# Kernel optimization log

Measured on AMD Instinct MI355X. Metric: run time of the kernel, lower is better.

The kernel has to match this reference:

```python
import jax, jax.numpy as jnp
import numpy as np

N_NODES = 10000
N_EDGES = 160000
MUL = 128            # channel multiplicity of node features
N_ELEM = 10          # node_attrs scalars (num elements)
N_EDGE_FEATS = 8     # radial basis size
W_NUMEL = 4 * MUL    # 4 uvu paths, 128 weights each
AVG_NEIGH = 16.0
INV_SQRT3 = 0.5773502691896258  # CG coefficient for 1o x 1o -> 0e (dot product path)


def setup_inputs() -> dict:
    key = jax.random.key(0)
    ks = jax.random.split(key, 12)
    node_attrs = jax.random.uniform(ks[0], (N_NODES, N_ELEM), dtype=jnp.float32)
    node_feats = jax.random.normal(ks[1], (N_NODES, MUL * 4), dtype=jnp.float32)  # 128x0e + 128x1o flattened
    edge_attrs = jax.random.normal(ks[2], (N_EDGES, 4), dtype=jnp.float32)        # Y0 (1) + Y1 (3)
    edge_feats = jax.random.normal(ks[3], (N_EDGES, N_EDGE_FEATS), dtype=jnp.float32)
    edge_index = jax.random.randint(ks[4], (2, N_EDGES), 0, N_NODES, dtype=jnp.int64)
    # learned parameters (xavier-ish scales; e3nn path norms folded into weights)
    W_up0 = jax.random.normal(ks[5], (MUL, MUL), dtype=jnp.float32) / np.sqrt(MUL)
    W_up1 = jax.random.normal(ks[6], (MUL, MUL), dtype=jnp.float32) / np.sqrt(MUL)
    W_tpw = jax.random.normal(ks[7], (N_ELEM, N_EDGE_FEATS, W_NUMEL), dtype=jnp.float32) / np.sqrt(N_ELEM * N_EDGE_FEATS)
    W_lin0 = jax.random.normal(ks[8], (2 * MUL, MUL), dtype=jnp.float32) / np.sqrt(2 * MUL)
    W_lin1 = jax.random.normal(ks[9], (2 * MUL, MUL), dtype=jnp.float32) / np.sqrt(2 * MUL)
    W_sk0 = jax.random.normal(ks[10], (MUL, N_ELEM, MUL), dtype=jnp.float32) / np.sqrt(MUL * N_ELEM)
    W_sk1 = jax.random.normal(ks[11], (MUL, N_ELEM, MUL), dtype=jnp.float32) / np.sqrt(MUL * N_ELEM)
    return dict(node_attrs=node_attrs, node_feats=node_feats, edge_attrs=edge_attrs,
                edge_feats=edge_feats, edge_index=edge_index,
                W_up0=W_up0, W_up1=W_up1, W_tpw=W_tpw,
                W_lin0=W_lin0, W_lin1=W_lin1, W_sk0=W_sk0, W_sk1=W_sk1)


def reference(node_attrs, node_feats, edge_attrs, edge_feats, edge_index,
              W_up0, W_up1, W_tpw, W_lin0, W_lin1, W_sk0, W_sk1):
    N = node_feats.shape[0]
    sender, receiver = edge_index[0], edge_index[1]
    x0 = node_feats[:, :MUL]                       # [N,128] scalars (0e)
    x1 = node_feats[:, MUL:].reshape(N, MUL, 3)    # [N,128,3] vectors (1o)

    # skip_tp: FullyConnectedTensorProduct(node_feats, node_attrs -> 128x0e+128x1o)
    sc0 = jnp.einsum('nu,na,uak->nk', x0, node_attrs, W_sk0)        # [N,128]
    sc1 = jnp.einsum('num,na,uak->nkm', x1, node_attrs, W_sk1)      # [N,128,3]

    # linear_up: per-l linear
    h0 = x0 @ W_up0                                   # [N,128]
    h1 = jnp.einsum('num,uk->nkm', x1, W_up1)         # [N,128,3]

    # per-edge TP weights: einsum('be,ba,aek->bk')
    tpw = jnp.einsum('be,ba,aek->bk', edge_feats, node_attrs[sender], W_tpw)  # [E,512]
    w1, w2, w3, w4 = tpw[:, :MUL], tpw[:, MUL:2*MUL], tpw[:, 2*MUL:3*MUL], tpw[:, 3*MUL:]

    Y0 = edge_attrs[:, 0]       # [E]
    Y1 = edge_attrs[:, 1:4]     # [E,3]
    hs0 = h0[sender]            # [E,128] gather
    hs1 = h1[sender]            # [E,128,3]

    # conv_tp (uvu, external per-edge weights), 4 CG paths:
    m0a = w1 * hs0 * Y0[:, None]                                       # 0e x 0e -> 0e
    m1a = (w2 * hs0)[:, :, None] * Y1[:, None, :]                      # 0e x 1o -> 1o
    m1b = hs1 * (w3 * Y0[:, None])[:, :, None]                         # 1o x 0e -> 1o
    m0b = w4 * (INV_SQRT3 * jnp.einsum('eum,em->eu', hs1, Y1))         # 1o x 1o -> 0e
    m0 = jnp.concatenate([m0a, m0b], axis=1)    # [E,256]  irreps_mid 0e block
    m1 = jnp.concatenate([m1a, m1b], axis=1)    # [E,256,3] irreps_mid 1o block

    # scatter_sum over receiver
    msg0 = jax.ops.segment_sum(m0, receiver, num_segments=N)   # [N,256]
    msg1 = jax.ops.segment_sum(m1, receiver, num_segments=N)   # [N,256,3]

    # linear (irreps_mid -> 128x0e+128x1o) / avg_num_neighbors + skip
    out0 = (msg0 @ W_lin0) / AVG_NEIGH + sc0                        # [N,128]
    out1 = jnp.einsum('num,uk->nkm', msg1, W_lin1) / AVG_NEIGH + sc1  # [N,128,3]
    return jnp.concatenate([out0, out1.reshape(N, MUL * 3)], axis=1)  # [N,512]
```

## Files before the change

kernel.cpp:

```cpp
#include <hip/hip_runtime.h>

#define NN 10000
#define NE 160000
#define NBK0 157
#define NBK1 469

constexpr float INV_AVG = 1.0f / 16.0f;
constexpr float INV_SQRT3F = 0.5773502691896258f;

typedef __attribute__((ext_vector_type(8))) short short8v;
typedef __attribute__((ext_vector_type(8))) unsigned short ushort8v;
typedef __attribute__((ext_vector_type(4))) float float4v;

#define OF_UP0 0
#define OF_UP1 16384
#define OF_SK0 32768
#define OF_SK1 196608
#define OF_LN0 360448
#define OF_LN1 393216
#define WPK_TOT 425984
#define WTP_TOT 49152

__device__ __forceinline__ unsigned short f2bf(float f) {
    unsigned int u = __float_as_uint(f);
    return (unsigned short)((u + 0x7FFFu + ((u >> 16) & 1u)) >> 16);
}
__device__ __forceinline__ float bf2f(unsigned short h) {
    return __uint_as_float(((unsigned int)h) << 16);
}

__global__ __launch_bounds__(256) void prep_w_kernel(
    const float* __restrict__ W_up0, const float* __restrict__ W_up1,
    const float* __restrict__ W_sk0, const float* __restrict__ W_sk1,
    const float* __restrict__ W_lin0, const float* __restrict__ W_lin1,
    unsigned short* __restrict__ wpk)
{
    const int g = blockIdx.x * 256 + threadIdx.x;
    if (g >= WPK_TOT / 8) return;
    const float* src; int local, base; bool sk = false;
    if (g < 2048)       { src = W_up0;  local = g;         base = OF_UP0; }
    else if (g < 4096)  { src = W_up1;  local = g - 2048;  base = OF_UP1; }
    else if (g < 24576) { src = W_sk0;  local = g - 4096;  base = OF_SK0; sk = true; }
    else if (g < 45056) { src = W_sk1;  local = g - 24576; base = OF_SK1; sk = true; }
    else if (g < 49152) { src = W_lin0; local = g - 45056; base = OF_LN0; }
    else                { src = W_lin1; local = g - 49152; base = OF_LN1; }
    const int k8 = local >> 7, n = local & 127;
    ushort8v v;
    #pragma unroll
    for (int j = 0; j < 8; ++j) {
        const int k = k8 * 8 + j;
        int row;
        if (sk) {
            const int a = k >> 7, u = k & 127;
            row = u * 10 + a;
        } else {
            row = k;
        }
        v[j] = f2bf(src[(size_t)row * 128 + n]);
    }
    *(ushort8v*)(wpk + (size_t)base + (size_t)local * 8) = v;
}

__global__ __launch_bounds__(256) void prep_wt_kernel(
    const float* __restrict__ W_tpw, unsigned short* __restrict__ wtp)
{
    const int g = blockIdx.x * 256 + threadIdx.x;
    if (g >= 6144) return;
    const int k8 = g >> 9, col = g & 511;
    ushort8v v;
    #pragma unroll
    for (int j = 0; j < 8; ++j) {
        const int k = k8 * 8 + j;
        v[j] = (k < 80) ? f2bf(W_tpw[(size_t)k * 512 + col]) : (unsigned short)0;
    }
    *(ushort8v*)(wtp + (size_t)g * 8) = v;
}

__global__ __launch_bounds__(256, 2) void node_mfma_kernel(
    const float* __restrict__ node_attrs,
    const float* __restrict__ node_feats,
    const unsigned short* __restrict__ wpk,
    float* __restrict__ hbuf,
    float* __restrict__ out)
{
    __shared__ __align__(16) unsigned short habuf[1024][8];
    __shared__ __align__(16) unsigned short bbuf[2][1024][8];
    __shared__ float atrow[64][10];

    const int t = threadIdx.x;
    const int bid = blockIdx.x;
    const bool m1 = (bid >= NBK0);
    const int r0 = m1 ? (bid - NBK0) * 64 : bid * 64;
    const int RTOT = m1 ? 30000 : 10000;

    const unsigned short* __restrict__ wup = wpk + (m1 ? OF_UP1 : OF_UP0);
    const unsigned short* __restrict__ wsk = wpk + (m1 ? OF_SK1 : OF_SK0);

    const int rg_ = t >> 2, pg_ = t & 3;
    const int rr_g = min(r0 + rg_, RTOT - 1);
    int n_g, m_g;
    if (!m1) { n_g = rr_g; m_g = 0; }
    else     { n_g = rr_g / 3; m_g = rr_g - n_g * 3; }
    const int wq = rg_ >> 4, rlq = rg_ & 15;

    #pragma unroll
    for (int q = 0; q < 4; ++q) {
        const int sl = pg_ * 4 + q, ss = sl >> 2, kb = sl & 3;
        const int k0 = ss * 32 + kb * 8;
        ushort8v v;
        if (!m1) {
            const float4 xa_ = *(const float4*)(node_feats + (size_t)n_g * 512 + k0);
            const float4 xb_ = *(const float4*)(node_feats + (size_t)n_g * 512 + k0 + 4);
            v[0] = f2bf(xa_.x); v[1] = f2bf(xa_.y); v[2] = f2bf(xa_.z); v[3] = f2bf(xa_.w);
            v[4] = f2bf(xb_.x); v[5] = f2bf(xb_.y); v[6] = f2bf(xb_.z); v[7] = f2bf(xb_.w);
        } else {
            #pragma unroll
            for (int j = 0; j < 8; ++j)
                v[j] = f2bf(node_feats[(size_t)n_g * 512 + 128 + (k0 + j) * 3 + m_g]);
        }
        *(ushort8v*)&habuf[((ss * 4 + wq) * 4 + kb) * 16 + rlq][0] = v;
    }
    for (int i = t; i < 640; i += 256) {
        const int r = i / 10, a = i - r * 10;
        const int rr = min(r0 + r, RTOT - 1);
        const int n = m1 ? (rr / 3) : rr;
        atrow[r][a] = node_attrs[n * 10 + a];
    }
    __syncthreads();

    const int w = t >> 6, lane = t & 63;
    const int rl = lane & 15, kq = lane >> 4;

    {
        float4v hacc[8];
        #pragma unroll
        for (int nt = 0; nt < 8; ++nt) hacc[nt] = (float4v){0.f, 0.f, 0.f, 0.f};

        #pragma unroll
        for (int ss = 0; ss < 4; ++ss) {
            const short8v af = *(const short8v*)&habuf[((ss * 4 + w) * 4 + kq) * 16 + rl][0];
            #pragma unroll
            for (int nt = 0; nt < 8; ++nt) {
                const short8v bf = *(const short8v*)(wup +
                    ((size_t)((ss * 4 + kq) * 128 + nt * 16 + rl)) * 8);
                hacc[nt] = __builtin_amdgcn_mfma_f32_16x16x32_bf16(af, bf, hacc[nt], 0, 0, 0);
            }
        }
        #pragma unroll
        for (int nt = 0; nt < 8; ++nt)
            #pragma unroll
            for (int v2 = 0; v2 < 4; ++v2) {
                const int rr = r0 + w * 16 + kq * 4 + v2;
                if (rr < RTOT) {
                    const int col = nt * 16 + rl;
                    if (!m1) hbuf[(size_t)rr * 512 + col] = hacc[nt][v2];
                    else {
                        const int n = rr / 3, m = rr - n * 3;
                        hbuf[(size_t)n * 512 + 128 + m * 128 + col] = hacc[nt][v2];
                    }
                }
            }
    }

    float4v sacc[8];
    #pragma unroll
    for (int nt = 0; nt < 8; ++nt) sacc[nt] = (float4v){0.f, 0.f, 0.f, 0.f};

    #pragma unroll
    for (int i = 0; i < 4; ++i) {
        const int s = i * 256 + t;
        const int ssb = s >> 9, ntb = (s >> 6) & 7, kbb = (s >> 4) & 3, nlb = s & 15;
        const int k8 = ssb * 4 + kbb;
        const int n = ntb * 16 + nlb;
        *(ushort8v*)&bbuf[0][s][0] =
            *(const ushort8v*)(wsk + ((size_t)(k8 * 128 + n)) * 8);
    }
    __syncthreads();

    int cur = 0;
    for (int ks = 0; ks < 20; ++ks) {
        ushort8v tmp[4];
        if (ks < 19) {
            #pragma unroll
            for (int i = 0; i < 4; ++i) {
                const int s = i * 256 + t;
                const int ssb = s >> 9, ntb = (s >> 6) & 7, kbb = (s >> 4) & 3, nlb = s & 15;
                const int k8 = (ks + 1) * 8 + ssb * 4 + kbb;
                const int n = ntb * 16 + nlb;
                tmp[i] = *(const ushort8v*)(wsk + ((size_t)(k8 * 128 + n)) * 8);
            }
        }

        short8v af[2];
        #pragma unroll
        for (int ss = 0; ss < 2; ++ss) {
            const int kp = ks * 64 + ss * 32 + kq * 8;
            const int a = kp >> 7, u0 = kp & 127;
            const ushort8v xh = *(const ushort8v*)&habuf[
                (((u0 >> 5) * 4 + w) * 4 + ((u0 >> 3) & 3)) * 16 + rl][0];
            const float av = atrow[w * 16 + rl][a];
            ushort8v vv;
            #pragma unroll
            for (int j = 0; j < 8; ++j) vv[j] = f2bf(bf2f(xh[j]) * av);
            af[ss] = (short8v)vv;
        }

        #pragma unroll
        for (int ss = 0; ss < 2; ++ss)
            #pragma unroll
            for (int nt = 0; nt < 8; ++nt) {
                const short8v bf =
                    *(const short8v*)&bbuf[cur][((ss * 8 + nt) * 4 + kq) * 16 + rl][0];
                sacc[nt] = __builtin_amdgcn_mfma_f32_16x16x32_bf16(af[ss], bf, sacc[nt], 0, 0, 0);
            }

        if (ks < 19) {
            #pragma unroll
            for (int i = 0; i < 4; ++i) {
                const int s = i * 256 + t;
                *(ushort8v*)&bbuf[cur ^ 1][s][0] = tmp[i];
            }
        }
        __syncthreads();
        cur ^= 1;
    }

    #pragma unroll
    for (int nt = 0; nt < 8; ++nt)
        #pragma unroll
        for (int v2 = 0; v2 < 4; ++v2) {
            const int rr = r0 + w * 16 + kq * 4 + v2;
            if (rr < RTOT) {
                const int col = nt * 16 + rl;
                if (!m1) out[(size_t)rr * 512 + col] = sacc[nt][v2];
                else {
                    const int n = rr / 3, m = rr - n * 3;
                    out[(size_t)n * 512 + 128 + col * 3 + m] = sacc[nt][v2];
                }
            }
        }
}

__global__ __launch_bounds__(256) void hist_kernel(
    const int* __restrict__ recv, int* __restrict__ cnt)
{
    const int e = blockIdx.x * 256 + threadIdx.x;
    if (e < NE) atomicAdd(&cnt[recv[e]], 1);
}

__global__ __launch_bounds__(256) void scan_kernel(
    const int* __restrict__ cnt, int* __restrict__ row_start,
    int* __restrict__ head)
{
    __shared__ int part[256];
    const int t = threadIdx.x;
    const int base = t * 40;
    int s = 0;
    if (base < NN)
        for (int b = 0; b < 40; ++b) s += cnt[base + b];
    part[t] = s;
    __syncthreads();
    const int local = s;
    for (int off = 1; off < 256; off <<= 1) {
        const int v = (t >= off) ? part[t - off] : 0;
        __syncthreads();
        part[t] += v;
        __syncthreads();
    }
    const int excl = part[t] - local;
    if (base < NN) {
        int run = excl;
        for (int b = 0; b < 40; ++b) {
            row_start[base + b] = run;
            head[base + b] = run;
            run += cnt[base + b];
        }
    }
    if (t == 0) row_start[NN] = NE;
}

__global__ __launch_bounds__(256) void scatter_kernel(
    const int* __restrict__ recv, int* __restrict__ head,
    int* __restrict__ elist)
{
    const int e = blockIdx.x * 256 + threadIdx.x;
    if (e < NE) {
        const int p = atomicAdd(&head[recv[e]], 1);
        elist[p] = e;
    }
}

__global__ __launch_bounds__(256) void pack2_kernel(
    const float* __restrict__ node_attrs,
    const float* __restrict__ edge_attrs,
    const float* __restrict__ edge_feats,
    const int*  __restrict__ edge_index,
    const int*  __restrict__ elist,
    unsigned short* __restrict__ zpk,
    float* __restrict__ ypk)
{
    const int pos = blockIdx.x * 256 + threadIdx.x;
    if (pos >= NE) return;
    const int e = elist[pos];
    const int snd = edge_index[e];

    float ef[8];
    *(float4*)&ef[0] = *(const float4*)(edge_feats + (size_t)e * 8);
    *(float4*)&ef[4] = *(const float4*)(edge_feats + (size_t)e * 8 + 4);
    float at[10];
    #pragma unroll
    for (int a = 0; a < 10; ++a) at[a] = node_attrs[(size_t)snd * 10 + a];

    #pragma unroll
    for (int k8 = 0; k8 < 12; ++k8) {
        ushort8v v;
        #pragma unroll
        for (int j = 0; j < 8; ++j) {
            const int A = k8 * 8 + j;
            const float z = (A < 80) ? at[A >> 3] * ef[A & 7] : 0.f;
            v[j] = f2bf(z);
        }
        *(ushort8v*)(zpk + ((size_t)k8 * NE + pos) * 8) = v;
    }

    const float4 ea = *(const float4*)(edge_attrs + (size_t)e * 4);
    *(float4*)(ypk + (size_t)pos * 8) = ea;
    *(float4*)(ypk + (size_t)pos * 8 + 4) =
        make_float4(__int_as_float(snd), 0.f, 0.f, 0.f);
}

__global__ __launch_bounds__(256, 2) void gather_mfma_kernel(
    const unsigned short* __restrict__ wtp,
    const float* __restrict__ hbuf,
    const int*  __restrict__ row_start,
    const unsigned short* __restrict__ zpk,
    const float* __restrict__ ypk,
    float* __restrict__ msgbuf)
{
    __shared__ __align__(16) unsigned short zb[384][8];
    __shared__ float yb[32][9];

    const int t = threadIdx.x;
    const int p = blockIdx.x & 1;
    const int ngrp = blockIdx.x >> 1;
    const int w = t >> 6, lane = t & 63;
    const int rl = lane & 15, kq = lane >> 4;

    short8v breg[2][3][2];
    #pragma unroll
    for (int wi = 0; wi < 2; ++wi)
        #pragma unroll
        for (int ks = 0; ks < 3; ++ks)
            #pragma unroll
            for (int ct = 0; ct < 2; ++ct) {
                const int col = p * 256 + wi * 128 + w * 32 + ct * 16 + rl;
                breg[wi][ks][ct] = *(const short8v*)(wtp +
                    ((size_t)((ks * 4 + kq) * 512 + col)) * 8);
            }

    for (int nn = 0; nn < 4; ++nn) {
        const int node = ngrp * 4 + nn;
        const int rowst = row_start[node];
        const int deg = row_start[node + 1] - rowst;

        float nacc[2][4];
        #pragma unroll
        for (int ct = 0; ct < 2; ++ct)
            #pragma unroll
            for (int j = 0; j < 4; ++j) nacc[ct][j] = 0.f;

        for (int ce = 0; ce < deg; ce += 32) {
            const int cl = min(32, deg - ce);
            __syncthreads();

            {
                const int s = t;
                const int rl2 = s & 15, kq2 = (s >> 4) & 3;
                const int rowt2 = (s >> 6) & 1, ks2 = s >> 7;
                const int e = rowt2 * 16 + rl2;
                const int k8 = ks2 * 4 + kq2;
                ushort8v v = {0, 0, 0, 0, 0, 0, 0, 0};
                if (e < cl)
                    v = *(const ushort8v*)(zpk + ((size_t)k8 * NE + rowst + ce + e) * 8);
                *(ushort8v*)&zb[s][0] = v;
            }
            {
                const int s = 256 + t;
                if (s < 384) {
                    const int rl2 = s & 15, kq2 = (s >> 4) & 3;
                    const int rowt2 = (s >> 6) & 1, ks2 = s >> 7;
                    const int e = rowt2 * 16 + rl2;
                    const int k8 = ks2 * 4 + kq2;
                    ushort8v v = {0, 0, 0, 0, 0, 0, 0, 0};
                    if (e < cl)
                        v = *(const ushort8v*)(zpk + ((size_t)k8 * NE + rowst + ce + e) * 8);
                    *(ushort8v*)&zb[s][0] = v;
                }
            }
            if (t < 64) {
                const int row = t >> 1, half = t & 1;
                float4 v = make_float4(0.f, 0.f, 0.f, 0.f);
                if (row < cl)
                    v = *(const float4*)(ypk + (size_t)(rowst + ce + row) * 8 + half * 4);
                yb[row][half * 4 + 0] = v.x;
                yb[row][half * 4 + 1] = v.y;
                yb[row][half * 4 + 2] = v.z;
                yb[row][half * 4 + 3] = v.w;
            }
            __syncthreads();

            if (p == 0) {
                #pragma unroll
                for (int rt = 0; rt < 2; ++rt) {
                    if (rt == 1 && cl <= 16) continue;
                    float h0v[4][2];
                    #pragma unroll
                    for (int v = 0; v < 4; ++v) {
                        const int e = rt * 16 + kq * 4 + v;
                        const int snd = __float_as_int(yb[e][4]);
                        const float* hrow = hbuf + (size_t)snd * 512;
                        #pragma unroll
                        for (int ct = 0; ct < 2; ++ct)
                            h0v[v][ct] = hrow[w * 32 + ct * 16 + rl];
                    }
                    float4v acc[2][2];
                    #pragma unroll
                    for (int wi = 0; wi < 2; ++wi)
                        #pragma unroll
                        for (int ct = 0; ct < 2; ++ct)
                            acc[wi][ct] = (float4v){0.f, 0.f, 0.f, 0.f};
                    #pragma unroll
                    for (int ks = 0; ks < 3; ++ks) {
                        const short8v af =
                            *(const short8v*)&zb[ks * 128 + rt * 64 + lane][0];
                        #pragma unroll
                        for (int wi = 0; wi < 2; ++wi)
                            #pragma unroll
                            for (int ct = 0; ct < 2; ++ct)
                                acc[wi][ct] = __builtin_amdgcn_mfma_f32_16x16x32_bf16(
                                    af, breg[wi][ks][ct], acc[wi][ct], 0, 0, 0);
                    }
                    #pragma unroll
                    for (int v = 0; v < 4; ++v) {
                        const int e = rt * 16 + kq * 4 + v;
                        const float Y0  = yb[e][0];
                        const float Y10 = yb[e][1];
                        const float Y11 = yb[e][2];
                        const float Y12 = yb[e][3];
                        #pragma unroll
                        for (int ct = 0; ct < 2; ++ct) {
                            const float tA = acc[0][ct][v];
                            const float tB = acc[1][ct][v];
                            const float h0 = h0v[v][ct];
                            nacc[ct][0] = fmaf(tA * Y0, h0, nacc[ct][0]);
                            const float tm = tB * h0;
                            nacc[ct][1] = fmaf(tm, Y10, nacc[ct][1]);
                            nacc[ct][2] = fmaf(tm, Y11, nacc[ct][2]);
                            nacc[ct][3] = fmaf(tm, Y12, nacc[ct][3]);
                        }
                    }
                }
            } else {
                #pragma unroll
                for (int rt = 0; rt < 2; ++rt) {
                    if (rt == 1 && cl <= 16) continue;
                    float hA[4][2], hB[4][2], hC[4][2];
                    #pragma unroll
                    for (int v = 0; v < 4; ++v) {
                        const int e = rt * 16 + kq * 4 + v;
                        const int snd = __float_as_int(yb[e][4]);
                        const float* hrow = hbuf + (size_t)snd * 512;
                        #pragma unroll
                        for (int ct = 0; ct < 2; ++ct) {
                            const int c = w * 32 + ct * 16 + rl;
                            hA[v][ct] = hrow[128 + c];
                            hB[v][ct] = hrow[256 + c];
                            hC[v][ct] = hrow[384 + c];
                        }
                    }
                    float4v acc[2][2];
                    #pragma unroll
                    for (int wi = 0; wi < 2; ++wi)
                        #pragma unroll
                        for (int ct = 0; ct < 2; ++ct)
                            acc[wi][ct] = (float4v){0.f, 0.f, 0.f, 0.f};
                    #pragma unroll
                    for (int ks = 0; ks < 3; ++ks) {
                        const short8v af =
                            *(const short8v*)&zb[ks * 128 + rt * 64 + lane][0];
                        #pragma unroll
                        for (int wi = 0; wi < 2; ++wi)
                            #pragma unroll
                            for (int ct = 0; ct < 2; ++ct)
                                acc[wi][ct] = __builtin_amdgcn_mfma_f32_16x16x32_bf16(
                                    af, breg[wi][ks][ct], acc[wi][ct], 0, 0, 0);
                    }
                    #pragma unroll
                    for (int v = 0; v < 4; ++v) {
                        const int e = rt * 16 + kq * 4 + v;
                        const float Y0  = yb[e][0];
                        const float Y10 = yb[e][1];
                        const float Y11 = yb[e][2];
                        const float Y12 = yb[e][3];
                        #pragma unroll
                        for (int ct = 0; ct < 2; ++ct) {
                            const float tA = acc[0][ct][v];
                            const float tB = acc[1][ct][v];
                            const float t2 = tA * Y0;
                            nacc[ct][1] = fmaf(t2, hA[v][ct], nacc[ct][1]);
                            nacc[ct][2] = fmaf(t2, hB[v][ct], nacc[ct][2]);
                            nacc[ct][3] = fmaf(t2, hC[v][ct], nacc[ct][3]);
                            float d = hA[v][ct] * Y10;
                            d = fmaf(hB[v][ct], Y11, d);
                            d = fmaf(hC[v][ct], Y12, d);
                            nacc[ct][0] = fmaf(tB * INV_SQRT3F, d, nacc[ct][0]);
                        }
                    }
                }
            }
        }

        float red[2][4];
        #pragma unroll
        for (int ct = 0; ct < 2; ++ct)
            #pragma unroll
            for (int j = 0; j < 4; ++j) {
                float v = nacc[ct][j];
                v += __shfl_xor(v, 16, 64);
                v += __shfl_xor(v, 32, 64);
                red[ct][j] = v;
            }
        if (kq == 0) {
            float* mrow = msgbuf + (size_t)node * 1024;
            #pragma unroll
            for (int ct = 0; ct < 2; ++ct) {
                const int c = w * 32 + ct * 16 + rl;
                if (p == 0) {
                    mrow[c]       = red[ct][0];
                    mrow[256 + c] = red[ct][1];
                    mrow[512 + c] = red[ct][2];
                    mrow[768 + c] = red[ct][3];
                } else {
                    mrow[128 + c] = red[ct][0];
                    mrow[384 + c] = red[ct][1];
                    mrow[640 + c] = red[ct][2];
                    mrow[896 + c] = red[ct][3];
                }
            }
        }
    }
}

__global__ __launch_bounds__(256, 2) void out_mfma_kernel(
    const float* __restrict__ msgbuf,
    const unsigned short* __restrict__ wpk,
    float* __restrict__ out)
{
    __shared__ __align__(16) unsigned short habuf[2048][8];

    const int t = threadIdx.x;
    const int n0 = blockIdx.x * 16;

    const int rg_ = t >> 2, pg_ = t & 3;
    const int wq = rg_ >> 4, rlq = rg_ & 15;
    const float* src = msgbuf + (size_t)(n0 + rlq) * 1024 + wq * 256;

    #pragma unroll
    for (int q = 0; q < 8; ++q) {
        const int sl = pg_ * 8 + q, ss = sl >> 2, kb = sl & 3;
        const int k0 = ss * 32 + kb * 8;
        const float4 xa = *(const float4*)(src + k0);
        const float4 xb = *(const float4*)(src + k0 + 4);
        ushort8v v;
        v[0] = f2bf(xa.x); v[1] = f2bf(xa.y); v[2] = f2bf(xa.z); v[3] = f2bf(xa.w);
        v[4] = f2bf(xb.x); v[5] = f2bf(xb.y); v[6] = f2bf(xb.z); v[7] = f2bf(xb.w);
        *(ushort8v*)&habuf[((ss * 4 + wq) * 4 + kb) * 16 + rlq][0] = v;
    }
    __syncthreads();

    const int w = t >> 6, lane = t & 63;
    const int rl = lane & 15, kq = lane >> 4;
    const unsigned short* __restrict__ wl = wpk + ((w == 0) ? OF_LN0 : OF_LN1);

    float4v acc[8];
    #pragma unroll
    for (int nt = 0; nt < 8; ++nt) acc[nt] = (float4v){0.f, 0.f, 0.f, 0.f};

    #pragma unroll
    for (int ss = 0; ss < 8; ++ss) {
        const short8v af = *(const short8v*)&habuf[((ss * 4 + w) * 4 + kq) * 16 + rl][0];
        #pragma unroll
        for (int nt = 0; nt < 8; ++nt) {
            const short8v bf = *(const short8v*)(wl +
                ((size_t)((ss * 4 + kq) * 128 + nt * 16 + rl)) * 8);
            acc[nt] = __builtin_amdgcn_mfma_f32_16x16x32_bf16(af, bf, acc[nt], 0, 0, 0);
        }
    }

    #pragma unroll
    for (int nt = 0; nt < 8; ++nt)
        #pragma unroll
        for (int v2 = 0; v2 < 4; ++v2) {
            const int n = n0 + kq * 4 + v2;
            const int col = nt * 16 + rl;
            if (w == 0) {
                out[(size_t)n * 512 + col] += acc[nt][v2] * INV_AVG;
            } else {
                const int m = w - 1;
                out[(size_t)n * 512 + 128 + col * 3 + m] += acc[nt][v2] * INV_AVG;
            }
        }
}

extern "C" void kernel_launch(void* const* d_in, const int* in_sizes, int n_in,
                              void* d_out, int out_size, void* d_ws, size_t ws_size,
                              hipStream_t stream) {
    const float* node_attrs = (const float*)d_in[0];
    const float* node_feats = (const float*)d_in[1];
    const float* edge_attrs = (const float*)d_in[2];
    const float* edge_feats = (const float*)d_in[3];
    const int*   edge_index = (const int*)d_in[4];
    const float* W_up0  = (const float*)d_in[5];
    const float* W_up1  = (const float*)d_in[6];
    const float* W_tpw  = (const float*)d_in[7];
    const float* W_lin0 = (const float*)d_in[8];
    const float* W_lin1 = (const float*)d_in[9];
    const float* W_sk0  = (const float*)d_in[10];
    const float* W_sk1  = (const float*)d_in[11];
    float* out = (float*)d_out;

    float* hbuf   = (float*)d_ws;
    float* msgbuf = hbuf + (size_t)NN * 512;
    float* ypk    = msgbuf + (size_t)NN * 1024;
    unsigned short* zpk = (unsigned short*)(ypk + (size_t)NE * 8);
    unsigned short* wpk = zpk + (size_t)12 * NE * 8;
    unsigned short* wtp = wpk + WPK_TOT;
    int* cnt       = (int*)(wtp + WTP_TOT);
    int* row_start = cnt + NN;
    int* head      = row_start + NN + 1;
    int* elist     = head + NN;

    const int* recv = edge_index + NE;

    hipMemsetAsync(cnt, 0, NN * sizeof(int), stream);
    hist_kernel<<<(NE + 255) / 256, 256, 0, stream>>>(recv, cnt);
    scan_kernel<<<1, 256, 0, stream>>>(cnt, row_start, head);
    scatter_kernel<<<(NE + 255) / 256, 256, 0, stream>>>(recv, head, elist);
    pack2_kernel<<<(NE + 255) / 256, 256, 0, stream>>>(
        node_attrs, edge_attrs, edge_feats, edge_index, elist, zpk, ypk);
    prep_w_kernel<<<(WPK_TOT / 8 + 255) / 256, 256, 0, stream>>>(
        W_up0, W_up1, W_sk0, W_sk1, W_lin0, W_lin1, wpk);
    prep_wt_kernel<<<24, 256, 0, stream>>>(W_tpw, wtp);

    node_mfma_kernel<<<NBK0 + NBK1, 256, 0, stream>>>(node_attrs, node_feats,
                                                      wpk, hbuf, out);
    gather_mfma_kernel<<<5000, 256, 0, stream>>>(wtp, hbuf, row_start,
                                                 zpk, ypk, msgbuf);
    out_mfma_kernel<<<NN / 16, 256, 0, stream>>>(msgbuf, wpk, out);
}
```

Baseline: 208.2 us.

## Double-buffer edge chunk staging in gather kernel to overlap loads with MFMA

Flattens the per-node, per-chunk loop of the gather kernel into one chunk stream over the block's four nodes. It double-buffers the zpk and ypk staging in LDS: the next chunk's global loads are issued into registers before the current chunk's MFMA and epilogue, then written to the alternate buffer. This cuts the syncs per chunk from two to one and hides global load latency behind compute. In exchange it doubles LDS use, adds register pressure from the prefetched values, and zero-degree nodes now need an explicit zero write.

```diff
diff --git a/kernel.cpp b/kernel.cpp
--- a/kernel.cpp
+++ b/kernel.cpp
@@ -50,12 +50,8 @@
     for (int j = 0; j < 8; ++j) {
         const int k = k8 * 8 + j;
         int row;
-        if (sk) {
-            const int a = k >> 7, u = k & 127;
-            row = u * 10 + a;
-        } else {
-            row = k;
-        }
+        if (sk) { const int a = k >> 7, u = k & 127; row = u * 10 + a; }
+        else    { row = k; }
         v[j] = f2bf(src[(size_t)row * 128 + n]);
     }
     *(ushort8v*)(wpk + (size_t)base + (size_t)local * 8) = v;
@@ -337,8 +333,8 @@
     const float* __restrict__ ypk,
     float* __restrict__ msgbuf)
 {
-    __shared__ __align__(16) unsigned short zb[384][8];
-    __shared__ float yb[32][9];
+    __shared__ __align__(16) unsigned short zb[2][384][8];
+    __shared__ float yb[2][32][9];
 
     const int t = threadIdx.x;
     const int p = blockIdx.x & 1;
@@ -346,6 +342,14 @@
     const int w = t >> 6, lane = t & 63;
     const int rl = lane & 15, kq = lane >> 4;
 
+    const int srl2 = t & 15, skq2 = (t >> 4) & 3;
+    const int srt2 = (t >> 6) & 1, sks2 = t >> 7;
+    const int se0 = srt2 * 16 + srl2, sk80 = sks2 * 4 + skq2;
+    const int s1 = 256 + t;
+    const int srl2b = s1 & 15, skq2b = (s1 >> 4) & 3;
+    const int srt2b = (s1 >> 6) & 1, sks2b = s1 >> 7;
+    const int se1 = srt2b * 16 + srl2b, sk81 = sks2b * 4 + skq2b;
+
     short8v breg[2][3][2];
     #pragma unroll
     for (int wi = 0; wi < 2; ++wi)
@@ -358,196 +362,254 @@
                     ((size_t)((ks * 4 + kq) * 512 + col)) * 8);
             }
 
-    for (int nn = 0; nn < 4; ++nn) {
-        const int node = ngrp * 4 + nn;
-        const int rowst = row_start[node];
-        const int deg = row_start[node + 1] - rowst;
-
-        float nacc[2][4];
-        #pragma unroll
-        for (int ct = 0; ct < 2; ++ct)
-            #pragma unroll
-            for (int j = 0; j < 4; ++j) nacc[ct][j] = 0.f;
-
-        for (int ce = 0; ce < deg; ce += 32) {
-            const int cl = min(32, deg - ce);
-            __syncthreads();
-
-            {
-                const int s = t;
-                const int rl2 = s & 15, kq2 = (s >> 4) & 3;
-                const int rowt2 = (s >> 6) & 1, ks2 = s >> 7;
-                const int e = rowt2 * 16 + rl2;
-                const int k8 = ks2 * 4 + kq2;
-                ushort8v v = {0, 0, 0, 0, 0, 0, 0, 0};
-                if (e < cl)
-                    v = *(const ushort8v*)(zpk + ((size_t)k8 * NE + rowst + ce + e) * 8);
-                *(ushort8v*)&zb[s][0] = v;
-            }
-            {
-                const int s = 256 + t;
-                if (s < 384) {
-                    const int rl2 = s & 15, kq2 = (s >> 4) & 3;
-                    const int rowt2 = (s >> 6) & 1, ks2 = s >> 7;
-                    const int e = rowt2 * 16 + rl2;
-                    const int k8 = ks2 * 4 + kq2;
-                    ushort8v v = {0, 0, 0, 0, 0, 0, 0, 0};
-                    if (e < cl)
-                        v = *(const ushort8v*)(zpk + ((size_t)k8 * NE + rowst + ce + e) * 8);
-                    *(ushort8v*)&zb[s][0] = v;
-                }
-            }
+    int rowsts[4], degs[4];
+    #pragma unroll
+    for (int i = 0; i < 4; ++i) {
+        const int node = ngrp * 4 + i;
+        rowsts[i] = row_start[node];
+        degs[i] = row_start[node + 1] - rowsts[i];
+    }
+
+    #pragma unroll
+    for (int i = 0; i < 4; ++i) {
+        if (degs[i] == 0 && kq == 0) {
+            float* mrow = msgbuf + (size_t)(ngrp * 4 + i) * 1024;
+            #pragma unroll
+            for (int ct = 0; ct < 2; ++ct) {
+                const int c = w * 32 + ct * 16 + rl;
+                if (p == 0) {
+                    mrow[c] = 0.f; mrow[256 + c] = 0.f;
+                    mrow[512 + c] = 0.f; mrow[768 + c] = 0.f;
+                } else {
+                    mrow[128 + c] = 0.f; mrow[384 + c] = 0.f;
+                    mrow[640 + c] = 0.f; mrow[896 + c] = 0.f;
+                }
+            }
+        }
+    }
+
+    int nn = 0;
+    while (nn < 4 && degs[nn] == 0) nn++;
+    int ce = 0;
+
+    if (nn < 4) {
+        const int cl0 = min(32, degs[nn]);
+        const int rowb = rowsts[nn];
+        {
+            ushort8v v = {0, 0, 0, 0, 0, 0, 0, 0};
+            if (se0 < cl0)
+                v = *(const ushort8v*)(zpk + ((size_t)sk80 * NE + rowb + se0) * 8);
+            *(ushort8v*)&zb[0][t][0] = v;
+        }
+        if (s1 < 384) {
+            ushort8v v = {0, 0, 0, 0, 0, 0, 0, 0};
+            if (se1 < cl0)
+                v = *(const ushort8v*)(zpk + ((size_t)sk81 * NE + rowb + se1) * 8);
+            *(ushort8v*)&zb[0][s1][0] = v;
+        }
+        if (t < 64) {
+            const int row = t >> 1, half = t & 1;
+            float4 v = make_float4(0.f, 0.f, 0.f, 0.f);
+            if (row < cl0)
+                v = *(const float4*)(ypk + (size_t)(rowb + row) * 8 + half * 4);
+            yb[0][row][half * 4 + 0] = v.x;
+            yb[0][row][half * 4 + 1] = v.y;
+            yb[0][row][half * 4 + 2] = v.z;
+            yb[0][row][half * 4 + 3] = v.w;
+        }
+    }
+    __syncthreads();
+
+    float nacc[2][4];
+    #pragma unroll
+    for (int ct = 0; ct < 2; ++ct)
+        #pragma unroll
+        for (int j = 0; j < 4; ++j) nacc[ct][j] = 0.f;
+
+    int cur = 0;
+    while (nn < 4) {
+        const int cl = min(32, degs[nn] - ce);
+
+        int nn2 = nn, ce2 = ce + 32;
+        if (ce2 >= degs[nn2]) {
+            do { nn2++; } while (nn2 < 4 && degs[nn2] == 0);
+            ce2 = 0;
+        }
+        const bool have2 = (nn2 < 4);
+
+        ushort8v zt0 = {0, 0, 0, 0, 0, 0, 0, 0};
+        ushort8v zt1 = {0, 0, 0, 0, 0, 0, 0, 0};
+        float4 yt = make_float4(0.f, 0.f, 0.f, 0.f);
+        if (have2) {
+            const int cl2 = min(32, degs[nn2] - ce2);
+            const int rowb = rowsts[nn2] + ce2;
+            if (se0 < cl2)
+                zt0 = *(const ushort8v*)(zpk + ((size_t)sk80 * NE + rowb + se0) * 8);
+            if (s1 < 384 && se1 < cl2)
+                zt1 = *(const ushort8v*)(zpk + ((size_t)sk81 * NE + rowb + se1) * 8);
             if (t < 64) {
                 const int row = t >> 1, half = t & 1;
-                float4 v = make_float4(0.f, 0.f, 0.f, 0.f);
-                if (row < cl)
-                    v = *(const float4*)(ypk + (size_t)(rowst + ce + row) * 8 + half * 4);
-                yb[row][half * 4 + 0] = v.x;
-                yb[row][half * 4 + 1] = v.y;
-                yb[row][half * 4 + 2] = v.z;
-                yb[row][half * 4 + 3] = v.w;
-            }
-            __syncthreads();
-
-            if (p == 0) {
-                #pragma unroll
-                for (int rt = 0; rt < 2; ++rt) {
-                    if (rt == 1 && cl <= 16) continue;
-                    float h0v[4][2];
+                if (row < cl2)
+                    yt = *(const float4*)(ypk + (size_t)(rowb + row) * 8 + half * 4);
+            }
+        }
+
+        if (p == 0) {
+            #pragma unroll
+            for (int rt = 0; rt < 2; ++rt) {
+                if (rt == 1 && cl <= 16) continue;
+                float h0v[4][2];
+                #pragma unroll
+                for (int v = 0; v < 4; ++v) {
+                    const int e = rt * 16 + kq * 4 + v;
+                    const int snd = __float_as_int(yb[cur][e][4]);
+                    const float* hrow = hbuf + (size_t)snd * 512;
                     #pragma unroll
-                    for (int v = 0; v < 4; ++v) {
-                        const int e = rt * 16 + kq * 4 + v;
-                        const int snd = __float_as_int(yb[e][4]);
-                        const float* hrow = hbuf + (size_t)snd * 512;
-                        #pragma unroll
-                        for (int ct = 0; ct < 2; ++ct)
-                            h0v[v][ct] = hrow[w * 32 + ct * 16 + rl];
-                    }
-                    float4v acc[2][2];
+                    for (int ct = 0; ct < 2; ++ct)
+                        h0v[v][ct] = hrow[w * 32 + ct * 16 + rl];
+                }
+                float4v acc[2][2];
+                #pragma unroll
+                for (int wi = 0; wi < 2; ++wi)
+                    #pragma unroll
+                    for (int ct = 0; ct < 2; ++ct)
+                        acc[wi][ct] = (float4v){0.f, 0.f, 0.f, 0.f};
+                #pragma unroll
+                for (int ks = 0; ks < 3; ++ks) {
+                    const short8v af =
+                        *(const short8v*)&zb[cur][ks * 128 + rt * 64 + lane][0];
                     #pragma unroll
                     for (int wi = 0; wi < 2; ++wi)
                         #pragma unroll
                         for (int ct = 0; ct < 2; ++ct)
-                            acc[wi][ct] = (float4v){0.f, 0.f, 0.f, 0.f};
+                            acc[wi][ct] = __builtin_amdgcn_mfma_f32_16x16x32_bf16(
+                                af, breg[wi][ks][ct], acc[wi][ct], 0, 0, 0);
+                }
+                #pragma unroll
+                for (int v = 0; v < 4; ++v) {
+                    const int e = rt * 16 + kq * 4 + v;
+                    const float Y0  = yb[cur][e][0];
+                    const float Y10 = yb[cur][e][1];
+                    const float Y11 = yb[cur][e][2];
+                    const float Y12 = yb[cur][e][3];
                     #pragma unroll
-                    for (int ks = 0; ks < 3; ++ks) {
-                        const short8v af =
-                            *(const short8v*)&zb[ks * 128 + rt * 64 + lane][0];
-                        #pragma unroll
-                        for (int wi = 0; wi < 2; ++wi)
-                            #pragma unroll
-                            for (int ct = 0; ct < 2; ++ct)
-                                acc[wi][ct] = __builtin_amdgcn_mfma_f32_16x16x32_bf16(
-                                    af, breg[wi][ks][ct], acc[wi][ct], 0, 0, 0);
+                    for (int ct = 0; ct < 2; ++ct) {
+                        const float tA = acc[0][ct][v];
+                        const float tB = acc[1][ct][v];
+                        const float h0 = h0v[v][ct];
+                        nacc[ct][0] = fmaf(tA * Y0, h0, nacc[ct][0]);
+                        const float tm = tB * h0;
+                        nacc[ct][1] = fmaf(tm, Y10, nacc[ct][1]);
+                        nacc[ct][2] = fmaf(tm, Y11, nacc[ct][2]);
+                        nacc[ct][3] = fmaf(tm, Y12, nacc[ct][3]);
                     }
+                }
+            }
+        } else {
+            #pragma unroll
+            for (int rt = 0; rt < 2; ++rt) {
+                if (rt == 1 && cl <= 16) continue;
+                float hA[4][2], hB[4][2], hC[4][2];
+                #pragma unroll
+                for (int v = 0; v < 4; ++v) {
+                    const int e = rt * 16 + kq * 4 + v;
+                    const int snd = __float_as_int(yb[cur][e][4]);
+                    const float* hrow = hbuf + (size_t)snd * 512;
                     #pragma unroll
-                    for (int v = 0; v < 4; ++v) {
-                        const int e = rt * 16 + kq * 4 + v;
-                        const float Y0  = yb[e][0];
-                        const float Y10 = yb[e][1];
-                        const float Y11 = yb[e][2];
-                        const float Y12 = yb[e][3];
-                        #pragma unroll
-                        for (int ct = 0; ct < 2; ++ct) {
-                            const float tA = acc[0][ct][v];
-                            const float tB = acc[1][ct][v];
-                            const float h0 = h0v[v][ct];
-                            nacc[ct][0] = fmaf(tA * Y0, h0, nacc[ct][0]);
-                            const float tm = tB * h0;
-                            nacc[ct][1] = fmaf(tm, Y10, nacc[ct][1]);
-                            nacc[ct][2] = fmaf(tm, Y11, nacc[ct][2]);
-                            nacc[ct][3] = fmaf(tm, Y12, nacc[ct][3]);
-                        }
+                    for (int ct = 0; ct < 2; ++ct) {
+                        const int c = w * 32 + ct * 16 + rl;
+                        hA[v][ct] = hrow[128 + c];
+                        hB[v][ct] = hrow[256 + c];
+                        hC[v][ct] = hrow[384 + c];
                     }
                 }
-            } else {
-                #pragma unroll
-                for (int rt = 0; rt < 2; ++rt) {
-                    if (rt == 1 && cl <= 16) continue;
-                    float hA[4][2], hB[4][2], hC[4][2];
+                float4v acc[2][2];
+                #pragma unroll
+                for (int wi = 0; wi < 2; ++wi)
                     #pragma unroll
-                    for (int v = 0; v < 4; ++v) {
-                        const int e = rt * 16 + kq * 4 + v;
-                        const int snd = __float_as_int(yb[e][4]);
-                        const float* hrow = hbuf + (size_t)snd * 512;
-                        #pragma unroll
-                        for (int ct = 0; ct < 2; ++ct) {
-                            const int c = w * 32 + ct * 16 + rl;
-                            hA[v][ct] = hrow[128 + c];
-                            hB[v][ct] = hrow[256 + c];
-                            hC[v][ct] = hrow[384 + c];
-                        }
-                    }
-                    float4v acc[2][2];
+                    for (int ct = 0; ct < 2; ++ct)
+                        acc[wi][ct] = (float4v){0.f, 0.f, 0.f, 0.f};
+                #pragma unroll
+                for (int ks = 0; ks < 3; ++ks) {
+                    const short8v af =
+                        *(const short8v*)&zb[cur][ks * 128 + rt * 64 + lane][0];
                     #pragma unroll
                     for (int wi = 0; wi < 2; ++wi)
                         #pragma unroll
                         for (int ct = 0; ct < 2; ++ct)
-                            acc[wi][ct] = (float4v){0.f, 0.f, 0.f, 0.f};
+                            acc[wi][ct] = __builtin_amdgcn_mfma_f32_16x16x32_bf16(
+                                af, breg[wi][ks][ct], acc[wi][ct], 0, 0, 0);
+                }
+                #pragma unroll
+                for (int v = 0; v < 4; ++v) {
+                    const int e = rt * 16 + kq * 4 + v;
+                    const float Y0  = yb[cur][e][0];
+                    const float Y10 = yb[cur][e][1];
+                    const float Y11 = yb[cur][e][2];
+                    const float Y12 = yb[cur][e][3];
                     #pragma unroll
-                    for (int ks = 0; ks < 3; ++ks) {
-                        const short8v af =
-                            *(const short8v*)&zb[ks * 128 + rt * 64 + lane][0];
-                        #pragma unroll
-                        for (int wi = 0; wi < 2; ++wi)
-                            #pragma unroll
-                            for (int ct = 0; ct < 2; ++ct)
-                                acc[wi][ct] = __builtin_amdgcn_mfma_f32_16x16x32_bf16(
-                                    af, breg[wi][ks][ct], acc[wi][ct], 0, 0, 0);
+                    for (int ct = 0; ct < 2; ++ct) {
+                        const float tA = acc[0][ct][v];
+                        const float tB = acc[1][ct][v];
+                        const float t2 = tA * Y0;
+                        nacc[ct][1] = fmaf(t2, hA[v][ct], nacc[ct][1]);
+                        nacc[ct][2] = fmaf(t2, hB[v][ct], nacc[ct][2]);
+                        nacc[ct][3] = fmaf(t2, hC[v][ct], nacc[ct][3]);
+                        float d = hA[v][ct] * Y10;
+                        d = fmaf(hB[v][ct], Y11, d);
+                        d = fmaf(hC[v][ct], Y12, d);
+                        nacc[ct][0] = fmaf(tB * INV_SQRT3F, d, nacc[ct][0]);
                     }
-                    #pragma unroll
-                    for (int v = 0; v < 4; ++v) {
-                        const int e = rt * 16 + kq * 4 + v;
-                        const float Y0  = yb[e][0];
-                        const float Y10 = yb[e][1];
-                        const float Y11 = yb[e][2];
-                        const float Y12 = yb[e][3];
-                        #pragma unroll
-                        for (int ct = 0; ct < 2; ++ct) {
-                            const float tA = acc[0][ct][v];
-                            const float tB = acc[1][ct][v];
-                            const float t2 = tA * Y0;
-                            nacc[ct][1] = fmaf(t2, hA[v][ct], nacc[ct][1]);
-                            nacc[ct][2] = fmaf(t2, hB[v][ct], nacc[ct][2]);
-                            nacc[ct][3] = fmaf(t2, hC[v][ct], nacc[ct][3]);
-                            float d = hA[v][ct] * Y10;
-                            d = fmaf(hB[v][ct], Y11, d);
-                            d = fmaf(hC[v][ct], Y12, d);
-                            nacc[ct][0] = fmaf(tB * INV_SQRT3F, d, nacc[ct][0]);
-                        }
+                }
+            }
+        }
+
+        if (ce + 32 >= degs[nn]) {
+            float red[2][4];
+            #pragma unroll
+            for (int ct = 0; ct < 2; ++ct)
+                #pragma unroll
+                for (int j = 0; j < 4; ++j) {
+                    float v = nacc[ct][j];
+                    v += __shfl_xor(v, 16, 64);
+                    v += __shfl_xor(v, 32, 64);
+                    red[ct][j] = v;
+                    nacc[ct][j] = 0.f;
+                }
+            if (kq == 0) {
+                float* mrow = msgbuf + (size_t)(ngrp * 4 + nn) * 1024;
+                #pragma unroll
+                for (int ct = 0; ct < 2; ++ct) {
+                    const int c = w * 32 + ct * 16 + rl;
+                    if (p == 0) {
+                        mrow[c]       = red[ct][0];
+                        mrow[256 + c] = red[ct][1];
+                        mrow[512 + c] = red[ct][2];
+                        mrow[768 + c] = red[ct][3];
+                    } else {
+                        mrow[128 + c] = red[ct][0];
+                        mrow[384 + c] = red[ct][1];
+                        mrow[640 + c] = red[ct][2];
+                        mrow[896 + c] = red[ct][3];
                     }
                 }
             }
         }
 
-        float red[2][4];
-        #pragma unroll
-        for (int ct = 0; ct < 2; ++ct)
-            #pragma unroll
-            for (int j = 0; j < 4; ++j) {
-                float v = nacc[ct][j];
-                v += __shfl_xor(v, 16, 64);
-                v += __shfl_xor(v, 32, 64);
-                red[ct][j] = v;
-            }
-        if (kq == 0) {
-            float* mrow = msgbuf + (size_t)node * 1024;
-            #pragma unroll
-            for (int ct = 0; ct < 2; ++ct) {
-                const int c = w * 32 + ct * 16 + rl;
-                if (p == 0) {
-                    mrow[c]       = red[ct][0];
-                    mrow[256 + c] = red[ct][1];
-                    mrow[512 + c] = red[ct][2];
-                    mrow[768 + c] = red[ct][3];
-                } else {
-                    mrow[128 + c] = red[ct][0];
-                    mrow[384 + c] = red[ct][1];
-                    mrow[640 + c] = red[ct][2];
-                    mrow[896 + c] = red[ct][3];
-                }
-            }
-        }
+        if (have2) {
+            *(ushort8v*)&zb[cur ^ 1][t][0] = zt0;
+            if (s1 < 384) *(ushort8v*)&zb[cur ^ 1][s1][0] = zt1;
+            if (t < 64) {
+                const int row = t >> 1, half = t & 1;
+                yb[cur ^ 1][row][half * 4 + 0] = yt.x;
+                yb[cur ^ 1][row][half * 4 + 1] = yt.y;
+                yb[cur ^ 1][row][half * 4 + 2] = yt.z;
+                yb[cur ^ 1][row][half * 4 + 3] = yt.w;
+            }
+        }
+        __syncthreads();
+        cur ^= 1;
+        nn = nn2; ce = ce2;
     }
 }
 
```

Result: slower. 220.9 us (+6.1%).
